# Performance work log

Hardware: AMD Instinct MI355X
Metric: run time of the kernel (lower is better)

The kernel has to match this reference:

```python
import jax, jax.numpy as jnp
import numpy as np

B, M, S = 4, 1024, 1024
D, H, FF = 1024, 16, 4096
NE, P = 128, 1
HD = D // H
EPS = 1e-5


def _layer_norm(x, g, b):
    mu = x.mean(-1, keepdims=True)
    var = ((x - mu) ** 2).mean(-1, keepdims=True)
    return (x - mu) * jax.lax.rsqrt(var + EPS) * g + b


def _mha(q_in, kv_in, in_w, in_b, out_w, out_b):
    # torch nn.MultiheadAttention: packed in_proj_weight [3D, D], y = x @ W.T + b
    wq, wk, wv = in_w[:D], in_w[D:2 * D], in_w[2 * D:]
    bq, bk, bv = in_b[:D], in_b[D:2 * D], in_b[2 * D:]
    q = (q_in @ wq.T + bq).reshape(q_in.shape[0], q_in.shape[1], H, HD)
    k = (kv_in @ wk.T + bk).reshape(kv_in.shape[0], kv_in.shape[1], H, HD)
    v = (kv_in @ wv.T + bv).reshape(kv_in.shape[0], kv_in.shape[1], H, HD)
    scores = jnp.einsum('bqhd,bkhd->bhqk', q, k) / jnp.sqrt(jnp.float32(HD))
    attn = jax.nn.softmax(scores, axis=-1)
    o = jnp.einsum('bhqk,bkhd->bqhd', attn, v).reshape(q_in.shape[0], q_in.shape[1], D)
    return o @ out_w.T + out_b


def _soft_moe(h, phi, exp_w, exp_b):
    # h: [b, m, FF]; phi: [FF, n, p]
    logits = jnp.einsum('bmd,dnp->bmnp', h, phi)
    dispatch = jax.nn.softmax(logits, axis=1)  # over tokens m
    b, m, n, p = logits.shape
    combine = jax.nn.softmax(logits.reshape(b, m, n * p), axis=-1).reshape(b, m, n, p)
    slots = jnp.einsum('bmd,bmnp->bnpd', h, dispatch)  # [b, n, p, FF]
    y = jnp.einsum('bnpd,ndo->bnpo', slots, exp_w) + exp_b[None, :, None, :]  # [b, n, p, D]
    return jnp.einsum('bnpo,bmnp->bmo', y, combine)


def setup_inputs() -> dict:
    key = jax.random.key(0)
    ks = jax.random.split(key, 16)
    sc = 0.02

    def rn(k, shape):
        return jax.random.normal(k, shape, jnp.float32) * sc

    return {
        'tgt': jax.random.normal(ks[0], (B, M, D), jnp.float32),
        'memory': jax.random.normal(ks[1], (B, S, D), jnp.float32),
        'sa_in_w': rn(ks[2], (3 * D, D)), 'sa_in_b': jnp.zeros((3 * D,), jnp.float32),
        'sa_out_w': rn(ks[3], (D, D)), 'sa_out_b': jnp.zeros((D,), jnp.float32),
        'ca_in_w': rn(ks[4], (3 * D, D)), 'ca_in_b': jnp.zeros((3 * D,), jnp.float32),
        'ca_out_w': rn(ks[5], (D, D)), 'ca_out_b': jnp.zeros((D,), jnp.float32),
        'norm1_g': jnp.ones((D,), jnp.float32), 'norm1_b': jnp.zeros((D,), jnp.float32),
        'norm2_g': jnp.ones((D,), jnp.float32), 'norm2_b': jnp.zeros((D,), jnp.float32),
        'norm3_g': jnp.ones((D,), jnp.float32), 'norm3_b': jnp.zeros((D,), jnp.float32),
        'lin_w': rn(ks[6], (FF, D)), 'lin_b': jnp.zeros((FF,), jnp.float32),
        'phi': rn(ks[7], (FF, NE, P)),
        'exp_w': rn(ks[8], (NE, FF, D)), 'exp_b': jnp.zeros((NE, D), jnp.float32),
    }


def reference(tgt, memory, sa_in_w, sa_in_b, sa_out_w, sa_out_b,
              ca_in_w, ca_in_b, ca_out_w, ca_out_b,
              norm1_g, norm1_b, norm2_g, norm2_b, norm3_g, norm3_b,
              lin_w, lin_b, phi, exp_w, exp_b):
    # post-norm (norm_first=False), dropout=0 (eval)
    x = tgt
    x = _layer_norm(x + _mha(x, x, sa_in_w, sa_in_b, sa_out_w, sa_out_b), norm1_g, norm1_b)
    x = _layer_norm(x + _mha(x, memory, ca_in_w, ca_in_b, ca_out_w, ca_out_b), norm2_g, norm2_b)
    h = jax.nn.relu(x @ lin_w.T + lin_b)  # [B, M, FF]
    ff = _soft_moe(h, phi, exp_w, exp_b)  # [B, M, D]
    x = _layer_norm(x + ff, norm3_g, norm3_b)
    return x
```

## Files before the change

### kernel.cpp

```cpp
#include <hip/hip_runtime.h>
#include <cstdint>
#include <cstddef>

typedef unsigned short u16;
typedef unsigned int   u32;
typedef short bf16x8 __attribute__((ext_vector_type(8)));
typedef float f32x4  __attribute__((ext_vector_type(4)));
typedef u16   u16x8  __attribute__((ext_vector_type(8)));
typedef u16   u16x4  __attribute__((ext_vector_type(4)));
typedef u16   u16x2  __attribute__((ext_vector_type(2)));

constexpr int B_  = 4;
constexpr int M_  = 1024;
constexpr int S_  = 1024;
constexpr int D_  = 1024;
constexpr int H_  = 16;
constexpr int FF_ = 4096;
constexpr int NE_ = 128;

__device__ __forceinline__ u16 f2bf(float f) {
    u32 u = __builtin_bit_cast(u32, f);
    u = (u + 0x7fffu + ((u >> 16) & 1u)) >> 16;
    return (u16)u;
}
__device__ __forceinline__ float bf2f(u16 u) {
    u32 x = ((u32)u) << 16;
    return __builtin_bit_cast(float, x);
}
__device__ __forceinline__ void gload_lds16(const u16* g, u16* l) {
    __builtin_amdgcn_global_load_lds(
        (const __attribute__((address_space(1))) u32*)g,
        (__attribute__((address_space(3))) u32*)l, 16, 0, 0);
}

template<int OUT_BF16, int RELU, int HAS_BIAS, int WRITE_HT>
__global__ __launch_bounds__(256) void gemm64_mfma(
    const u16* __restrict__ A, const u16* __restrict__ W,
    const float* __restrict__ bias, void* __restrict__ Cout,
    u16* __restrict__ HT,
    int K, int N, int lda, int ldw,
    size_t sA, size_t sW, size_t sC)
{
    __shared__ u16 As[2][64 * 32];
    __shared__ u16 Bs[2][128 * 32];
    const int tid = threadIdx.x;
    const int w = tid >> 6, l = tid & 63;
    const int fr = l & 15, g = l >> 4;
    const int bm = blockIdx.y * 64, bn = blockIdx.x * 128;
    const u16* Ab = A + (size_t)blockIdx.z * sA;
    const u16* Wb = W + (size_t)blockIdx.z * sW;

    const int qcol = ((l & 3) ^ ((l >> 3) & 3)) * 8;
    const int srow = w * 16 + (l >> 2);
    const u16* aG  = Ab + (size_t)(bm + srow) * lda + qcol;
    const u16* bG0 = Wb + (size_t)(bn + srow) * ldw + qcol;
    const u16* bG1 = bG0 + (size_t)64 * ldw;
    const int wo = w * 512;

    const int qsw = (g ^ ((fr >> 1) & 3)) * 8;

    f32x4 acc[4][2];
#pragma unroll
    for (int m = 0; m < 4; ++m)
#pragma unroll
        for (int n = 0; n < 2; ++n)
#pragma unroll
            for (int q = 0; q < 4; ++q) acc[m][n][q] = 0.f;

    for (int k0 = 0; k0 < K; k0 += 64) {
        __syncthreads();
        gload_lds16(aG,       &As[0][wo]);
        gload_lds16(bG0,      &Bs[0][wo]);
        gload_lds16(bG1,      &Bs[0][2048 + wo]);
        gload_lds16(aG  + 32, &As[1][wo]);
        gload_lds16(bG0 + 32, &Bs[1][wo]);
        gload_lds16(bG1 + 32, &Bs[1][2048 + wo]);
        aG += 64; bG0 += 64; bG1 += 64;
        __syncthreads();
#pragma unroll
        for (int h = 0; h < 2; ++h) {
            bf16x8 af[4], bf[2];
#pragma unroll
            for (int m = 0; m < 4; ++m)
                af[m] = *(const bf16x8*)&As[h][(m * 16 + fr) * 32 + qsw];
#pragma unroll
            for (int n = 0; n < 2; ++n)
                bf[n] = *(const bf16x8*)&Bs[h][(w * 32 + n * 16 + fr) * 32 + qsw];
#pragma unroll
            for (int m = 0; m < 4; ++m)
#pragma unroll
                for (int n = 0; n < 2; ++n)
                    acc[m][n] = __builtin_amdgcn_mfma_f32_16x16x32_bf16(
                        af[m], bf[n], acc[m][n], 0, 0, 0);
        }
    }

    const int row0 = bm + g * 4;
#pragma unroll
    for (int n = 0; n < 2; ++n) {
        const int col = bn + w * 32 + n * 16 + fr;
        float bv = 0.f;
        if (HAS_BIAS) bv = bias[col];
#pragma unroll
        for (int m = 0; m < 4; ++m) {
            const int rowm = row0 + m * 16;
            u16 o[4];
#pragma unroll
            for (int j = 0; j < 4; ++j) {
                float v = acc[m][n][j] + bv;
                if (RELU) v = fmaxf(v, 0.f);
                const size_t idx = (size_t)blockIdx.z * sC +
                                   (size_t)(rowm + j) * N + col;
                if (OUT_BF16) { o[j] = f2bf(v); ((u16*)Cout)[idx] = o[j]; }
                else          { ((float*)Cout)[idx] = v; }
            }
            if (WRITE_HT) {
                u16x4 pk; pk[0] = o[0]; pk[1] = o[1]; pk[2] = o[2]; pk[3] = o[3];
                *(u16x4*)&HT[(((size_t)(rowm >> 10)) * N + col) * 1024 + (rowm & 1023)] = pk;
            }
        }
    }
}

__global__ __launch_bounds__(512) void flash_attn_kernel(
    const u16* __restrict__ Q, int qs,
    const u16* __restrict__ K, int ks,
    const u16* __restrict__ V, int vs,
    u16* __restrict__ O, int Slen)
{
    __shared__ u16 Ks[2][64][72];
    __shared__ u16 Vt[2][64][72];
    __shared__ u16 Pw[8][16][72];
    const int b = blockIdx.z, hh = blockIdx.y;
    const int m0 = blockIdx.x * 128;
    const int tid = threadIdx.x;
    const int w = tid >> 6, l = tid & 63;
    const int lq = l & 15, g = l >> 4;

    bf16x8 qf[2];
    {
        const u16* qp = Q + ((size_t)b * M_ + m0 + w * 16 + lq) * qs + hh * 64;
        u16x8 v0 = *(const u16x8*)(qp + g * 8);
        u16x8 v1 = *(const u16x8*)(qp + 32 + g * 8);
        u16x8 o0, o1;
#pragma unroll
        for (int i = 0; i < 8; ++i) {
            o0[i] = f2bf(bf2f(v0[i]) * 0.125f);
            o1[i] = f2bf(bf2f(v1[i]) * 0.125f);
        }
        qf[0] = __builtin_bit_cast(bf16x8, o0);
        qf[1] = __builtin_bit_cast(bf16x8, o1);
    }

    f32x4 acc_o[4];
#pragma unroll
    for (int nb = 0; nb < 4; ++nb)
#pragma unroll
        for (int j = 0; j < 4; ++j) acc_o[nb][j] = 0.f;
    float m_run = -1e30f, l_run = 0.f;

    const int krow = tid >> 3, kcg = (tid & 7) * 8;
    const int kp = tid & 31, dg = (tid >> 5) & 7;
    const int vstage = (tid < 256);

    const int nt = Slen >> 6;
    u16x8 kv0, va, vb;

#define ATT_LOAD(T_)                                                          \
    {                                                                         \
        const u16* kpp = K + ((size_t)b * Slen + (T_) * 64 + krow) * ks + hh * 64 + kcg; \
        kv0 = *(const u16x8*)kpp;                                             \
        if (vstage) {                                                         \
            const u16* vp0 = V + ((size_t)b * Slen + (T_) * 64 + 2 * kp) * vs + hh * 64 + dg * 8; \
            va = *(const u16x8*)vp0;                                          \
            vb = *(const u16x8*)(vp0 + vs);                                   \
        }                                                                     \
    }
#define ATT_WRITE(BUF_)                                                       \
    {                                                                         \
        *(u16x8*)&Ks[BUF_][krow][kcg] = kv0;                                  \
        if (vstage) {                                                         \
            _Pragma("unroll") for (int i = 0; i < 8; ++i) {                   \
                u16x2 pk; pk[0] = va[i]; pk[1] = vb[i];                       \
                *(u16x2*)&Vt[BUF_][dg * 8 + i][2 * kp] = pk;                  \
            }                                                                 \
        }                                                                     \
    }

    ATT_LOAD(0)
    ATT_WRITE(0)
    __syncthreads();

    for (int t = 0; t < nt; ++t) {
        if (t + 1 < nt) ATT_LOAD(t + 1)
        const int cb = t & 1;

        f32x4 s4[4];
#pragma unroll
        for (int mb = 0; mb < 4; ++mb) {
            f32x4 z = {0.f, 0.f, 0.f, 0.f};
            bf16x8 a0 = *(const bf16x8*)&Ks[cb][mb * 16 + lq][g * 8];
            bf16x8 a1 = *(const bf16x8*)&Ks[cb][mb * 16 + lq][32 + g * 8];
            z = __builtin_amdgcn_mfma_f32_16x16x32_bf16(a0, qf[0], z, 0, 0, 0);
            z = __builtin_amdgcn_mfma_f32_16x16x32_bf16(a1, qf[1], z, 0, 0, 0);
            s4[mb] = z;
        }

        float pm = -1e30f;
#pragma unroll
        for (int mb = 0; mb < 4; ++mb)
#pragma unroll
            for (int j = 0; j < 4; ++j) pm = fmaxf(pm, s4[mb][j]);
        pm = fmaxf(pm, __shfl_xor(pm, 16));
        pm = fmaxf(pm, __shfl_xor(pm, 32));

        u16 pbf[4][4];
        float ls = 0.f;
        if (__all(pm - m_run <= 8.f)) {
#pragma unroll
            for (int mb = 0; mb < 4; ++mb)
#pragma unroll
                for (int j = 0; j < 4; ++j) {
                    float p = __expf(s4[mb][j] - m_run);
                    ls += p;
                    pbf[mb][j] = f2bf(p);
                }
            ls += __shfl_xor(ls, 16);
            ls += __shfl_xor(ls, 32);
            l_run += ls;
        } else {
            const float m_new = fmaxf(m_run, pm);
            const float alpha = __expf(m_run - m_new);
#pragma unroll
            for (int mb = 0; mb < 4; ++mb)
#pragma unroll
                for (int j = 0; j < 4; ++j) {
                    float p = __expf(s4[mb][j] - m_new);
                    ls += p;
                    pbf[mb][j] = f2bf(p);
                }
            ls += __shfl_xor(ls, 16);
            ls += __shfl_xor(ls, 32);
            l_run = l_run * alpha + ls;
            m_run = m_new;
            float al[4];
#pragma unroll
            for (int j = 0; j < 4; ++j) al[j] = __shfl(alpha, 4 * g + j);
#pragma unroll
            for (int nb = 0; nb < 4; ++nb)
#pragma unroll
                for (int j = 0; j < 4; ++j) acc_o[nb][j] *= al[j];
        }

#pragma unroll
        for (int mb = 0; mb < 4; ++mb) {
            u16x4 pk;
            pk[0] = pbf[mb][0]; pk[1] = pbf[mb][1];
            pk[2] = pbf[mb][2]; pk[3] = pbf[mb][3];
            *(u16x4*)&Pw[w][lq][mb * 16 + g * 4] = pk;
        }

#pragma unroll
        for (int kc = 0; kc < 2; ++kc) {
            bf16x8 pa = *(const bf16x8*)&Pw[w][lq][kc * 32 + g * 8];
#pragma unroll
            for (int nb = 0; nb < 4; ++nb) {
                bf16x8 bv = *(const bf16x8*)&Vt[cb][nb * 16 + lq][kc * 32 + g * 8];
                acc_o[nb] = __builtin_amdgcn_mfma_f32_16x16x32_bf16(pa, bv, acc_o[nb], 0, 0, 0);
            }
        }

        if (t + 1 < nt) ATT_WRITE((t + 1) & 1)
        __syncthreads();
    }
#undef ATT_LOAD
#undef ATT_WRITE

    float linv[4];
#pragma unroll
    for (int j = 0; j < 4; ++j) linv[j] = 1.f / __shfl(l_run, 4 * g + j);
#pragma unroll
    for (int nb = 0; nb < 4; ++nb)
#pragma unroll
        for (int j = 0; j < 4; ++j) {
            const size_t row = (size_t)b * M_ + m0 + w * 16 + 4 * g + j;
            O[row * D_ + hh * 64 + nb * 16 + lq] = f2bf(acc_o[nb][j] * linv[j]);
        }
}

__global__ __launch_bounds__(256) void cvt_multi_kernel(
    const float* __restrict__ s0, u16* __restrict__ d0,
    const float* __restrict__ s1, u16* __restrict__ d1,
    const float* __restrict__ s2, u16* __restrict__ d2,
    const float* __restrict__ s3, u16* __restrict__ d3,
    const float* __restrict__ s4, u16* __restrict__ d4,
    const float* __restrict__ s5, u16* __restrict__ d5,
    const float* __restrict__ s6, u16* __restrict__ d6)
{
    int blk = blockIdx.x;
    const float* s; u16* d;
    if      (blk < 2048) { s = s0; d = d0; }
    else if (blk < 4096) { s = s1; d = d1; blk -= 2048; }
    else if (blk < 5632) { s = s2; d = d2; blk -= 4096; }
    else if (blk < 6144) { s = s3; d = d3; blk -= 5632; }
    else if (blk < 7680) { s = s4; d = d4; blk -= 6144; }
    else if (blk < 8192) { s = s5; d = d5; blk -= 7680; }
    else                 { s = s6; d = d6; blk -= 8192; }
    const size_t i = ((size_t)blk * 256 + threadIdx.x) * 8;
    float4 a = *(const float4*)(s + i);
    float4 b = *(const float4*)(s + i + 4);
    u16x8 o;
    o[0] = f2bf(a.x); o[1] = f2bf(a.y); o[2] = f2bf(a.z); o[3] = f2bf(a.w);
    o[4] = f2bf(b.x); o[5] = f2bf(b.y); o[6] = f2bf(b.z); o[7] = f2bf(b.w);
    *(u16x8*)(d + i) = o;
}

__global__ __launch_bounds__(256) void transpose_f32_bf16_kernel(
    const float* __restrict__ src, u16* __restrict__ dst, int R, int C,
    size_t sI, size_t sO)
{
    __shared__ u16 t[32][33];
    src += (size_t)blockIdx.z * sI;
    dst += (size_t)blockIdx.z * sO;
    const int c0 = blockIdx.x * 32, r0 = blockIdx.y * 32;
    const int x = threadIdx.x & 31, y = threadIdx.x >> 5;
    for (int i = y; i < 32; i += 8)
        t[i][x] = f2bf(src[(size_t)(r0 + i) * C + c0 + x]);
    __syncthreads();
    for (int i = y; i < 32; i += 8)
        dst[(size_t)(c0 + i) * R + r0 + x] = t[x][i];
}

template<int X_BF16, int OUT_F32>
__global__ __launch_bounds__(256) void resid_ln_kernel(
    const void* __restrict__ X, const u16* __restrict__ Rb,
    const float* __restrict__ g, const float* __restrict__ bt,
    void* __restrict__ Yout)
{
    __shared__ float s1[4], s2[4];
    const size_t row = blockIdx.x;
    const int tid = threadIdx.x;
    float xv[4];
    if (X_BF16) {
        u16x4 x4 = *(const u16x4*)((const u16*)X + row * 1024 + tid * 4);
#pragma unroll
        for (int i = 0; i < 4; ++i) xv[i] = bf2f(x4[i]);
    } else {
        float4 x4 = *(const float4*)((const float*)X + row * 1024 + tid * 4);
        xv[0] = x4.x; xv[1] = x4.y; xv[2] = x4.z; xv[3] = x4.w;
    }
    u16x4 r4 = *(const u16x4*)(Rb + row * 1024 + tid * 4);
    float v[4];
#pragma unroll
    for (int i = 0; i < 4; ++i) v[i] = xv[i] + bf2f(r4[i]);
    float s = v[0] + v[1] + v[2] + v[3];
    float q = v[0] * v[0] + v[1] * v[1] + v[2] * v[2] + v[3] * v[3];
#pragma unroll
    for (int off = 32; off; off >>= 1) {
        s += __shfl_xor(s, off);
        q += __shfl_xor(q, off);
    }
    if ((tid & 63) == 0) { s1[tid >> 6] = s; s2[tid >> 6] = q; }
    __syncthreads();
    s = s1[0] + s1[1] + s1[2] + s1[3];
    q = s2[0] + s2[1] + s2[2] + s2[3];
    const float mu = s * (1.f / 1024.f);
    const float var = q * (1.f / 1024.f) - mu * mu;
    const float rinv = rsqrtf(var + 1e-5f);
    const float4 g4 = *(const float4*)(g + tid * 4);
    const float4 b4 = *(const float4*)(bt + tid * 4);
    float o[4];
    o[0] = (v[0] - mu) * rinv * g4.x + b4.x;
    o[1] = (v[1] - mu) * rinv * g4.y + b4.y;
    o[2] = (v[2] - mu) * rinv * g4.z + b4.z;
    o[3] = (v[3] - mu) * rinv * g4.w + b4.w;
    if (OUT_F32) {
        *(float4*)((float*)Yout + row * 1024 + tid * 4) = *(float4*)o;
    } else {
        u16x4 ob;
        ob[0] = f2bf(o[0]); ob[1] = f2bf(o[1]);
        ob[2] = f2bf(o[2]); ob[3] = f2bf(o[3]);
        *(u16x4*)((u16*)Yout + row * 1024 + tid * 4) = ob;
    }
}

__global__ __launch_bounds__(256) void dispatch_softmax_T_kernel(
    const float* __restrict__ logitsP, u16* __restrict__ dispT)
{
    __shared__ float red[4];
    constexpr size_t CH = (size_t)B_ * M_ * NE_;
    const int n = blockIdx.x, b = blockIdx.y;
    u16* O = dispT + ((size_t)b * NE_ + n) * M_;
    const int tid = threadIdx.x;
    float v[4];
#pragma unroll
    for (int i = 0; i < 4; ++i) {
        const size_t idx = (size_t)(b * M_ + tid + 256 * i) * NE_ + n;
        v[i] = logitsP[idx] + logitsP[CH + idx] + logitsP[2 * CH + idx] + logitsP[3 * CH + idx];
    }
    float mx = fmaxf(fmaxf(v[0], v[1]), fmaxf(v[2], v[3]));
#pragma unroll
    for (int off = 32; off; off >>= 1) mx = fmaxf(mx, __shfl_xor(mx, off));
    if ((tid & 63) == 0) red[tid >> 6] = mx;
    __syncthreads();
    mx = fmaxf(fmaxf(red[0], red[1]), fmaxf(red[2], red[3]));
    __syncthreads();
    float e[4], s = 0.f;
#pragma unroll
    for (int i = 0; i < 4; ++i) { e[i] = __expf(v[i] - mx); s += e[i]; }
#pragma unroll
    for (int off = 32; off; off >>= 1) s += __shfl_xor(s, off);
    if ((tid & 63) == 0) red[tid >> 6] = s;
    __syncthreads();
    s = red[0] + red[1] + red[2] + red[3];
    const float inv = 1.f / s;
#pragma unroll
    for (int i = 0; i < 4; ++i) O[tid + 256 * i] = f2bf(e[i] * inv);
}

__global__ __launch_bounds__(64) void combine_softmax_kernel(
    const float* __restrict__ logitsP, u16* __restrict__ comb)
{
    constexpr size_t CH = (size_t)B_ * M_ * NE_;
    const size_t row = blockIdx.x;
    const int lane = threadIdx.x;
    const size_t i0 = row * NE_ + lane;
    const size_t i1 = i0 + 64;
    float a = logitsP[i0] + logitsP[CH + i0] + logitsP[2 * CH + i0] + logitsP[3 * CH + i0];
    float c = logitsP[i1] + logitsP[CH + i1] + logitsP[2 * CH + i1] + logitsP[3 * CH + i1];
    float mx = fmaxf(a, c);
#pragma unroll
    for (int off = 32; off; off >>= 1) mx = fmaxf(mx, __shfl_xor(mx, off));
    float e0 = __expf(a - mx), e1 = __expf(c - mx);
    float s = e0 + e1;
#pragma unroll
    for (int off = 32; off; off >>= 1) s += __shfl_xor(s, off);
    const float inv = 1.f / s;
    comb[row * NE_ + lane]      = f2bf(e0 * inv);
    comb[row * NE_ + lane + 64] = f2bf(e1 * inv);
}

__global__ __launch_bounds__(256) void expert_partial_kernel(
    const float* __restrict__ slots, const float* __restrict__ exp_w,
    float* __restrict__ part)
{
    __shared__ float sl[4][512];
    const int n = blockIdx.x;
    const int c = blockIdx.y;
    const int f0 = c * 512;
    const int t = threadIdx.x;
    for (int i = t; i < 2048; i += 256) {
        const int b = i >> 9, f = i & 511;
        sl[b][f] = slots[((size_t)b * NE_ + n) * FF_ + f0 + f];
    }
    __syncthreads();
    const int d4 = t * 4;
    const float* wp = exp_w + ((size_t)n * FF_ + f0) * D_ + d4;
    f32x4 acc[4];
#pragma unroll
    for (int b = 0; b < 4; ++b)
#pragma unroll
        for (int j = 0; j < 4; ++j) acc[b][j] = 0.f;
#pragma unroll 4
    for (int f = 0; f < 512; ++f) {
        const float4 w4 = *(const float4*)wp;
        wp += D_;
#pragma unroll
        for (int b = 0; b < 4; ++b) {
            const float s = sl[b][f];
            acc[b][0] = fmaf(s, w4.x, acc[b][0]);
            acc[b][1] = fmaf(s, w4.y, acc[b][1]);
            acc[b][2] = fmaf(s, w4.z, acc[b][2]);
            acc[b][3] = fmaf(s, w4.w, acc[b][3]);
        }
    }
#pragma unroll
    for (int b = 0; b < 4; ++b)
        *(f32x4*)&part[(((size_t)c * 4 + b) * NE_ + n) * D_ + d4] = acc[b];
}

__global__ __launch_bounds__(256) void reduce_yT_kernel(
    const float* __restrict__ part, const float* __restrict__ exp_b,
    u16* __restrict__ yT)
{
    __shared__ float tile[32][33];
    const int d0 = blockIdx.x * 32, n0 = blockIdx.y * 32, b = blockIdx.z;
    const int x = threadIdx.x & 31, y = threadIdx.x >> 5;
    for (int i = y; i < 32; i += 8) {
        const int n = n0 + i;
        float s = exp_b[(size_t)n * D_ + d0 + x];
#pragma unroll
        for (int c = 0; c < 8; ++c)
            s += part[(((size_t)c * 4 + b) * NE_ + n) * D_ + d0 + x];
        tile[i][x] = s;
    }
    __syncthreads();
    for (int i = y; i < 32; i += 8)
        yT[((size_t)b * D_ + d0 + i) * NE_ + n0 + x] = f2bf(tile[x][i]);
}

extern "C" void kernel_launch(void* const* d_in, const int* in_sizes, int n_in,
                              void* d_out, int out_size, void* d_ws, size_t ws_size,
                              hipStream_t stream)
{
    const float* tgt      = (const float*)d_in[0];
    const float* memry    = (const float*)d_in[1];
    const float* sa_in_w  = (const float*)d_in[2];
    const float* sa_in_b  = (const float*)d_in[3];
    const float* sa_out_w = (const float*)d_in[4];
    const float* sa_out_b = (const float*)d_in[5];
    const float* ca_in_w  = (const float*)d_in[6];
    const float* ca_in_b  = (const float*)d_in[7];
    const float* ca_out_w = (const float*)d_in[8];
    const float* ca_out_b = (const float*)d_in[9];
    const float* norm1_g  = (const float*)d_in[10];
    const float* norm1_b  = (const float*)d_in[11];
    const float* norm2_g  = (const float*)d_in[12];
    const float* norm2_b  = (const float*)d_in[13];
    const float* norm3_g  = (const float*)d_in[14];
    const float* norm3_b  = (const float*)d_in[15];
    const float* lin_w    = (const float*)d_in[16];
    const float* lin_b    = (const float*)d_in[17];
    const float* phi      = (const float*)d_in[18];
    const float* exp_w    = (const float*)d_in[19];
    const float* exp_b    = (const float*)d_in[20];

    float* ws = (float*)d_ws;
    u16*   qkv_bf  = (u16*)(ws);
    u16*   proj_bf = (u16*)(ws + 6291456);
    float* logitsP = ws + 18874368;
    float* part    = ws + 20971520;
    u16*   h_bf    = (u16*)(ws + 25165824);
    u16*   hT_bf   = (u16*)(ws + 33554432);
    u16*   obuf_bf = (u16*)(ws + 41943040);
    u16*   x1_bf   = (u16*)(ws + 44040192);
    u16*   x2_bf   = (u16*)(ws + 46137344);
    u16*   tgt_bf  = (u16*)(ws + 48234496);
    u16*   mem_bf  = (u16*)(ws + 50331648);
    u16*   dispT   = (u16*)(ws + 52428800);
    u16*   comb_bf = (u16*)(ws + 52690944);
    u16*   yT_bf   = (u16*)(ws + 52953088);
    float* slots   = ws + 53215232;
    u16*   w_sa_in = (u16*)(ws + 55312384);
    u16*   w_sa_out= (u16*)(ws + 56885248);
    u16*   w_ca_in = (u16*)(ws + 57409536);
    u16*   w_ca_out= (u16*)(ws + 58982400);
    u16*   w_lin   = (u16*)(ws + 59506688);
    u16*   phiT    = (u16*)(ws + 61603840);

    constexpr size_t CH = (size_t)B_ * M_ * NE_;

    cvt_multi_kernel<<<10240, 256, 0, stream>>>(
        tgt, tgt_bf, memry, mem_bf, sa_in_w, w_sa_in, sa_out_w, w_sa_out,
        ca_in_w, w_ca_in, ca_out_w, w_ca_out, lin_w, w_lin);
    transpose_f32_bf16_kernel<<<dim3(4, 128, 1), 256, 0, stream>>>(phi, phiT, 4096, 128, 0, 0);

    gemm64_mfma<1, 0, 1, 0><<<dim3(24, 64, 1), 256, 0, stream>>>(
        tgt_bf, w_sa_in, sa_in_b, qkv_bf, nullptr, 1024, 3072, 1024, 1024, 0, 0, 0);
    flash_attn_kernel<<<dim3(8, 16, 4), 512, 0, stream>>>(
        qkv_bf, 3072, qkv_bf + 1024, 3072, qkv_bf + 2048, 3072, obuf_bf, S_);
    gemm64_mfma<1, 0, 1, 0><<<dim3(8, 64, 1), 256, 0, stream>>>(
        obuf_bf, w_sa_out, sa_out_b, proj_bf, nullptr, 1024, 1024, 1024, 1024, 0, 0, 0);
    resid_ln_kernel<0, 0><<<4096, 256, 0, stream>>>(tgt, proj_bf, norm1_g, norm1_b, x1_bf);

    u16* qca_bf = qkv_bf;
    u16* kvca_bf = qkv_bf + (size_t)4096 * 1024;
    gemm64_mfma<1, 0, 1, 0><<<dim3(8, 64, 1), 256, 0, stream>>>(
        x1_bf, w_ca_in, ca_in_b, qca_bf, nullptr, 1024, 1024, 1024, 1024, 0, 0, 0);
    gemm64_mfma<1, 0, 1, 0><<<dim3(16, 64, 1), 256, 0, stream>>>(
        mem_bf, w_ca_in + (size_t)1024 * 1024, ca_in_b + 1024,
        kvca_bf, nullptr, 1024, 2048, 1024, 1024, 0, 0, 0);
    flash_attn_kernel<<<dim3(8, 16, 4), 512, 0, stream>>>(
        qca_bf, 1024, kvca_bf, 2048, kvca_bf + 1024, 2048, obuf_bf, S_);
    gemm64_mfma<1, 0, 1, 0><<<dim3(8, 64, 1), 256, 0, stream>>>(
        obuf_bf, w_ca_out, ca_out_b, proj_bf, nullptr, 1024, 1024, 1024, 1024, 0, 0, 0);
    resid_ln_kernel<1, 0><<<4096, 256, 0, stream>>>(x1_bf, proj_bf, norm2_g, norm2_b, x2_bf);

    gemm64_mfma<1, 1, 1, 1><<<dim3(32, 64, 1), 256, 0, stream>>>(
        x2_bf, w_lin, lin_b, h_bf, hT_bf, 1024, 4096, 1024, 1024, 0, 0, 0);
    gemm64_mfma<0, 0, 0, 0><<<dim3(1, 64, 4), 256, 0, stream>>>(
        h_bf, phiT, nullptr, logitsP, nullptr, 1024, 128, 4096, 4096,
        1024, 1024, CH);
    dispatch_softmax_T_kernel<<<dim3(NE_, B_), 256, 0, stream>>>(logitsP, dispT);
    combine_softmax_kernel<<<dim3(B_ * M_), 64, 0, stream>>>(logitsP, comb_bf);
    gemm64_mfma<0, 0, 0, 0><<<dim3(32, 2, 4), 256, 0, stream>>>(
        dispT, hT_bf, nullptr, slots, nullptr, 1024, 4096, 1024, 1024,
        (size_t)NE_ * M_, (size_t)FF_ * M_, (size_t)NE_ * FF_);
    expert_partial_kernel<<<dim3(NE_, 8), 256, 0, stream>>>(slots, exp_w, part);
    reduce_yT_kernel<<<dim3(32, 4, 4), 256, 0, stream>>>(part, exp_b, yT_bf);
    gemm64_mfma<1, 0, 0, 0><<<dim3(8, 16, 4), 256, 0, stream>>>(
        comb_bf, yT_bf, nullptr, proj_bf, nullptr, 128, 1024, 128, 128,
        (size_t)M_ * NE_, (size_t)D_ * NE_, (size_t)M_ * D_);
    resid_ln_kernel<1, 1><<<4096, 256, 0, stream>>>(x2_bf, proj_bf, norm3_g, norm3_b,
                                                    (float*)d_out);
}
```

Before: 748.1 us.

## Double-buffer GEMM K loop and merge small launches into fused kernels

The GEMM main loop now prefetches the next 32-wide K slice into the alternate LDS buffer while MFMAs run on the current one, with one barrier per step instead of two per 64-wide step. The phi transpose is folded into the bulk conversion kernel as extra blocks, and the dispatch and combine softmax kernels are merged into one launch. The goal is to hide global-to-LDS load latency and cut launch overhead. Risks include the LDS write into the other buffer racing with reads from the previous iteration, and halving the K work per barrier, which may reduce MFMA density.

Measured after the change: 759.1 us. Within noise of the previous version (+1.5%).

```diff
diff --git a/kernel.cpp b/kernel.cpp
--- a/kernel.cpp
+++ b/kernel.cpp
@@ -67,32 +67,36 @@
 #pragma unroll
             for (int q = 0; q < 4; ++q) acc[m][n][q] = 0.f;
 
-    for (int k0 = 0; k0 < K; k0 += 64) {
+    const int nt = K >> 5;
+    gload_lds16(aG,  &As[0][wo]);
+    gload_lds16(bG0, &Bs[0][wo]);
+    gload_lds16(bG1, &Bs[0][2048 + wo]);
+    aG += 32; bG0 += 32; bG1 += 32;
+    __syncthreads();
+
+    for (int t = 0; t < nt; ++t) {
+        const int cur = t & 1;
+        if (t + 1 < nt) {
+            const int nxt = cur ^ 1;
+            gload_lds16(aG,  &As[nxt][wo]);
+            gload_lds16(bG0, &Bs[nxt][wo]);
+            gload_lds16(bG1, &Bs[nxt][2048 + wo]);
+            aG += 32; bG0 += 32; bG1 += 32;
+        }
+        bf16x8 af[4], bf[2];
+#pragma unroll
+        for (int m = 0; m < 4; ++m)
+            af[m] = *(const bf16x8*)&As[cur][(m * 16 + fr) * 32 + qsw];
+#pragma unroll
+        for (int n = 0; n < 2; ++n)
+            bf[n] = *(const bf16x8*)&Bs[cur][(w * 32 + n * 16 + fr) * 32 + qsw];
+#pragma unroll
+        for (int m = 0; m < 4; ++m)
+#pragma unroll
+            for (int n = 0; n < 2; ++n)
+                acc[m][n] = __builtin_amdgcn_mfma_f32_16x16x32_bf16(
+                    af[m], bf[n], acc[m][n], 0, 0, 0);
         __syncthreads();
-        gload_lds16(aG,       &As[0][wo]);
-        gload_lds16(bG0,      &Bs[0][wo]);
-        gload_lds16(bG1,      &Bs[0][2048 + wo]);
-        gload_lds16(aG  + 32, &As[1][wo]);
-        gload_lds16(bG0 + 32, &Bs[1][wo]);
-        gload_lds16(bG1 + 32, &Bs[1][2048 + wo]);
-        aG += 64; bG0 += 64; bG1 += 64;
-        __syncthreads();
-#pragma unroll
-        for (int h = 0; h < 2; ++h) {
-            bf16x8 af[4], bf[2];
-#pragma unroll
-            for (int m = 0; m < 4; ++m)
-                af[m] = *(const bf16x8*)&As[h][(m * 16 + fr) * 32 + qsw];
-#pragma unroll
-            for (int n = 0; n < 2; ++n)
-                bf[n] = *(const bf16x8*)&Bs[h][(w * 32 + n * 16 + fr) * 32 + qsw];
-#pragma unroll
-            for (int m = 0; m < 4; ++m)
-#pragma unroll
-                for (int n = 0; n < 2; ++n)
-                    acc[m][n] = __builtin_amdgcn_mfma_f32_16x16x32_bf16(
-                        af[m], bf[n], acc[m][n], 0, 0, 0);
-        }
     }
 
     const int row0 = bm + g * 4;
@@ -295,9 +299,22 @@
     const float* __restrict__ s3, u16* __restrict__ d3,
     const float* __restrict__ s4, u16* __restrict__ d4,
     const float* __restrict__ s5, u16* __restrict__ d5,
-    const float* __restrict__ s6, u16* __restrict__ d6)
-{
+    const float* __restrict__ s6, u16* __restrict__ d6,
+    const float* __restrict__ phi, u16* __restrict__ phiT)
+{
+    __shared__ u16 t[32][33];
     int blk = blockIdx.x;
+    if (blk >= 10240) {
+        const int b2 = blk - 10240;
+        const int c0 = (b2 & 3) * 32, r0 = (b2 >> 2) * 32;
+        const int x = threadIdx.x & 31, y = threadIdx.x >> 5;
+        for (int i = y; i < 32; i += 8)
+            t[i][x] = f2bf(phi[(size_t)(r0 + i) * 128 + c0 + x]);
+        __syncthreads();
+        for (int i = y; i < 32; i += 8)
+            phiT[(size_t)(c0 + i) * 4096 + r0 + x] = t[x][i];
+        return;
+    }
     const float* s; u16* d;
     if      (blk < 2048) { s = s0; d = d0; }
     else if (blk < 4096) { s = s1; d = d1; blk -= 2048; }
@@ -313,22 +330,6 @@
     o[0] = f2bf(a.x); o[1] = f2bf(a.y); o[2] = f2bf(a.z); o[3] = f2bf(a.w);
     o[4] = f2bf(b.x); o[5] = f2bf(b.y); o[6] = f2bf(b.z); o[7] = f2bf(b.w);
     *(u16x8*)(d + i) = o;
-}
-
-__global__ __launch_bounds__(256) void transpose_f32_bf16_kernel(
-    const float* __restrict__ src, u16* __restrict__ dst, int R, int C,
-    size_t sI, size_t sO)
-{
-    __shared__ u16 t[32][33];
-    src += (size_t)blockIdx.z * sI;
-    dst += (size_t)blockIdx.z * sO;
-    const int c0 = blockIdx.x * 32, r0 = blockIdx.y * 32;
-    const int x = threadIdx.x & 31, y = threadIdx.x >> 5;
-    for (int i = y; i < 32; i += 8)
-        t[i][x] = f2bf(src[(size_t)(r0 + i) * C + c0 + x]);
-    __syncthreads();
-    for (int i = y; i < 32; i += 8)
-        dst[(size_t)(c0 + i) * R + r0 + x] = t[x][i];
 }
 
 template<int X_BF16, int OUT_F32>
@@ -384,60 +385,61 @@
     }
 }
 
-__global__ __launch_bounds__(256) void dispatch_softmax_T_kernel(
-    const float* __restrict__ logitsP, u16* __restrict__ dispT)
+__global__ __launch_bounds__(256) void moe_softmax_kernel(
+    const float* __restrict__ logitsP, u16* __restrict__ dispT,
+    u16* __restrict__ comb)
 {
     __shared__ float red[4];
     constexpr size_t CH = (size_t)B_ * M_ * NE_;
-    const int n = blockIdx.x, b = blockIdx.y;
-    u16* O = dispT + ((size_t)b * NE_ + n) * M_;
+    const int b = blockIdx.y;
     const int tid = threadIdx.x;
-    float v[4];
-#pragma unroll
-    for (int i = 0; i < 4; ++i) {
-        const size_t idx = (size_t)(b * M_ + tid + 256 * i) * NE_ + n;
-        v[i] = logitsP[idx] + logitsP[CH + idx] + logitsP[2 * CH + idx] + logitsP[3 * CH + idx];
-    }
-    float mx = fmaxf(fmaxf(v[0], v[1]), fmaxf(v[2], v[3]));
-#pragma unroll
-    for (int off = 32; off; off >>= 1) mx = fmaxf(mx, __shfl_xor(mx, off));
-    if ((tid & 63) == 0) red[tid >> 6] = mx;
-    __syncthreads();
-    mx = fmaxf(fmaxf(red[0], red[1]), fmaxf(red[2], red[3]));
-    __syncthreads();
-    float e[4], s = 0.f;
-#pragma unroll
-    for (int i = 0; i < 4; ++i) { e[i] = __expf(v[i] - mx); s += e[i]; }
-#pragma unroll
-    for (int off = 32; off; off >>= 1) s += __shfl_xor(s, off);
-    if ((tid & 63) == 0) red[tid >> 6] = s;
-    __syncthreads();
-    s = red[0] + red[1] + red[2] + red[3];
-    const float inv = 1.f / s;
-#pragma unroll
-    for (int i = 0; i < 4; ++i) O[tid + 256 * i] = f2bf(e[i] * inv);
-}
-
-__global__ __launch_bounds__(64) void combine_softmax_kernel(
-    const float* __restrict__ logitsP, u16* __restrict__ comb)
-{
-    constexpr size_t CH = (size_t)B_ * M_ * NE_;
-    const size_t row = blockIdx.x;
-    const int lane = threadIdx.x;
-    const size_t i0 = row * NE_ + lane;
-    const size_t i1 = i0 + 64;
-    float a = logitsP[i0] + logitsP[CH + i0] + logitsP[2 * CH + i0] + logitsP[3 * CH + i0];
-    float c = logitsP[i1] + logitsP[CH + i1] + logitsP[2 * CH + i1] + logitsP[3 * CH + i1];
-    float mx = fmaxf(a, c);
-#pragma unroll
-    for (int off = 32; off; off >>= 1) mx = fmaxf(mx, __shfl_xor(mx, off));
-    float e0 = __expf(a - mx), e1 = __expf(c - mx);
-    float s = e0 + e1;
-#pragma unroll
-    for (int off = 32; off; off >>= 1) s += __shfl_xor(s, off);
-    const float inv = 1.f / s;
-    comb[row * NE_ + lane]      = f2bf(e0 * inv);
-    comb[row * NE_ + lane + 64] = f2bf(e1 * inv);
+    if ((int)blockIdx.x < NE_) {
+        const int n = blockIdx.x;
+        u16* O = dispT + ((size_t)b * NE_ + n) * M_;
+        float v[4];
+#pragma unroll
+        for (int i = 0; i < 4; ++i) {
+            const size_t idx = (size_t)(b * M_ + tid + 256 * i) * NE_ + n;
+            v[i] = logitsP[idx] + logitsP[CH + idx] + logitsP[2 * CH + idx] + logitsP[3 * CH + idx];
+        }
+        float mx = fmaxf(fmaxf(v[0], v[1]), fmaxf(v[2], v[3]));
+#pragma unroll
+        for (int off = 32; off; off >>= 1) mx = fmaxf(mx, __shfl_xor(mx, off));
+        if ((tid & 63) == 0) red[tid >> 6] = mx;
+        __syncthreads();
+        mx = fmaxf(fmaxf(red[0], red[1]), fmaxf(red[2], red[3]));
+        __syncthreads();
+        float e[4], s = 0.f;
+#pragma unroll
+        for (int i = 0; i < 4; ++i) { e[i] = __expf(v[i] - mx); s += e[i]; }
+#pragma unroll
+        for (int off = 32; off; off >>= 1) s += __shfl_xor(s, off);
+        if ((tid & 63) == 0) red[tid >> 6] = s;
+        __syncthreads();
+        s = red[0] + red[1] + red[2] + red[3];
+        const float inv = 1.f / s;
+#pragma unroll
+        for (int i = 0; i < 4; ++i) O[tid + 256 * i] = f2bf(e[i] * inv);
+    } else {
+        const int idx4 = blockIdx.x - NE_;
+        const int m = idx4 * 4 + (tid >> 6);
+        const int lane = tid & 63;
+        const size_t row = (size_t)b * M_ + m;
+        const size_t i0 = row * NE_ + lane;
+        const size_t i1 = i0 + 64;
+        float a = logitsP[i0] + logitsP[CH + i0] + logitsP[2 * CH + i0] + logitsP[3 * CH + i0];
+        float c = logitsP[i1] + logitsP[CH + i1] + logitsP[2 * CH + i1] + logitsP[3 * CH + i1];
+        float mx = fmaxf(a, c);
+#pragma unroll
+        for (int off = 32; off; off >>= 1) mx = fmaxf(mx, __shfl_xor(mx, off));
+        float e0 = __expf(a - mx), e1 = __expf(c - mx);
+        float s = e0 + e1;
+#pragma unroll
+        for (int off = 32; off; off >>= 1) s += __shfl_xor(s, off);
+        const float inv = 1.f / s;
+        comb[row * NE_ + lane]      = f2bf(e0 * inv);
+        comb[row * NE_ + lane + 64] = f2bf(e1 * inv);
+    }
 }
 
 __global__ __launch_bounds__(256) void expert_partial_kernel(
@@ -550,10 +552,9 @@
 
     constexpr size_t CH = (size_t)B_ * M_ * NE_;
 
-    cvt_multi_kernel<<<10240, 256, 0, stream>>>(
+    cvt_multi_kernel<<<10752, 256, 0, stream>>>(
         tgt, tgt_bf, memry, mem_bf, sa_in_w, w_sa_in, sa_out_w, w_sa_out,
-        ca_in_w, w_ca_in, ca_out_w, w_ca_out, lin_w, w_lin);
-    transpose_f32_bf16_kernel<<<dim3(4, 128, 1), 256, 0, stream>>>(phi, phiT, 4096, 128, 0, 0);
+        ca_in_w, w_ca_in, ca_out_w, w_ca_out, lin_w, w_lin, phi, phiT);
 
     gemm64_mfma<1, 0, 1, 0><<<dim3(24, 64, 1), 256, 0, stream>>>(
         tgt_bf, w_sa_in, sa_in_b, qkv_bf, nullptr, 1024, 3072, 1024, 1024, 0, 0, 0);
@@ -581,8 +582,7 @@
     gemm64_mfma<0, 0, 0, 0><<<dim3(1, 64, 4), 256, 0, stream>>>(
         h_bf, phiT, nullptr, logitsP, nullptr, 1024, 128, 4096, 4096,
         1024, 1024, CH);
-    dispatch_softmax_T_kernel<<<dim3(NE_, B_), 256, 0, stream>>>(logitsP, dispT);
-    combine_softmax_kernel<<<dim3(B_ * M_), 64, 0, stream>>>(logitsP, comb_bf);
+    moe_softmax_kernel<<<dim3(NE_ + 256, B_), 256, 0, stream>>>(logitsP, dispT, comb_bf);
     gemm64_mfma<0, 0, 0, 0><<<dim3(32, 2, 4), 256, 0, stream>>>(
         dispT, hT_bf, nullptr, slots, nullptr, 1024, 4096, 1024, 1024,
         (size_t)NE_ * M_, (size_t)FF_ * M_, (size_t)NE_ * FF_);
```
